# Kernel optimization log

Hardware: AMD Instinct MI355X
Metric: run time of the kernel (lower is better)

The kernel has to match this reference:

```python
import jax, jax.numpy as jnp
import numpy as np

# TT factorization of a 4096 -> 4096 linear layer
IN_SHAPE = (8, 8, 8, 8)    # input_tt_shape, prod = 4096
OUT_SHAPE = (8, 8, 8, 8)   # output_tt_shape, prod = 4096
RANKS = (1, 16, 16, 16, 1) # tt_ranks, len = n_dim + 1
N_DIM = len(IN_SHAPE)
BATCH = 2048
OUT_SIZE = int(np.prod(OUT_SHAPE))
IN_SIZE = int(np.prod(IN_SHAPE))


def setup_inputs() -> dict:
    key = jax.random.key(0)
    ks = jax.random.split(key, N_DIM + 1)
    x = jax.random.normal(ks[0], (BATCH, IN_SIZE), dtype=jnp.float32)
    inp = {"x": x}
    for i in range(N_DIM):
        rows = RANKS[i] * OUT_SHAPE[i]
        cols = IN_SHAPE[i] * RANKS[i + 1]
        # xavier_uniform scale, matching torch init statistics
        limit = float(np.sqrt(6.0 / (rows + cols)))
        inp[f"core{i}"] = jax.random.uniform(
            ks[i + 1], (rows, cols), minval=-limit, maxval=limit, dtype=jnp.float32
        )
    inp["bias"] = jnp.zeros((OUT_SIZE,), dtype=jnp.float32)
    return inp


def reference(x, core0, core1, core2, core3, bias):
    cores = [core0, core1, core2, core3]
    res = x  # [B, prod(IN_SHAPE)]
    # Sequential TT-core contraction, last mode first (faithful to torch loop)
    for k in range(N_DIM - 1, -1, -1):
        res = res.reshape(-1, IN_SHAPE[k])                     # [.., n_k]
        res = res.T                                            # [n_k, ..]
        res = res.reshape(RANKS[k + 1] * IN_SHAPE[k], -1)      # [r_{k+1}*n_k, ..]
        res = cores[k] @ res                                   # [r_k*m_k, ..]
    res = res.reshape(OUT_SIZE, -1).T                          # [B, prod(OUT_SHAPE)]
    return res + bias
```

## Files before the change

### kernel.cpp

```cpp
#include <hip/hip_runtime.h>
#include <hip/hip_bf16.h>
#include <stdint.h>


typedef __bf16 bf16_t;
typedef __bf16 bf16x8 __attribute__((ext_vector_type(8)));
typedef __bf16 bf16x4 __attribute__((ext_vector_type(4)));
typedef float floatx4 __attribute__((ext_vector_type(4)));

#define BATCH_N 2048
#define KD 4096
#define ND 4096

__device__ static inline void load_lds16(const void* g, void* l) {
    __builtin_amdgcn_global_load_lds(
        (const __attribute__((address_space(1))) void*)g,
        (__attribute__((address_space(3))) void*)l, 16, 0, 0);
}

__global__ __launch_bounds__(256) void prep0(const float* __restrict__ x,
                                             const float* __restrict__ c0,
                                             const float* __restrict__ c1,
                                             const float* __restrict__ c2,
                                             const float* __restrict__ c3,
                                             bf16_t* __restrict__ xb,
                                             float* __restrict__ Pg,
                                             float* __restrict__ Tg) {
    const int t = threadIdx.x;
    const int b = blockIdx.x;

    if (b < 4096) {
        int g = b * 256 + t;
        const float4* xv = (const float4*)x;
        float4 a = xv[g * 2];
        float4 c = xv[g * 2 + 1];
        bf16x8 o;
        o[0] = (bf16_t)a.x; o[1] = (bf16_t)a.y; o[2] = (bf16_t)a.z; o[3] = (bf16_t)a.w;
        o[4] = (bf16_t)c.x; o[5] = (bf16_t)c.y; o[6] = (bf16_t)c.z; o[7] = (bf16_t)c.w;
        ((bf16x8*)xb)[g] = o;
        return;
    }

    __shared__ float s0[128];
    __shared__ float s1[2048];

    if (b < 4160) {
        const int n01 = b - 4096, n0 = n01 >> 3, n1 = n01 & 7;
        if (t < 128) s0[t] = c0[(t >> 4) * 128 + n0 * 16 + (t & 15)];
        for (int i = t; i < 2048; i += 256) {
            int r1 = i >> 7, m1 = (i >> 4) & 7, r2 = i & 15;
            s1[i] = c1[(r1 * 8 + m1) * 128 + n1 * 16 + r2];
        }
        __syncthreads();
#pragma unroll
        for (int j = 0; j < 4; ++j) {
            int o = j * 256 + t, m01 = o >> 4, r2 = o & 15;
            int m0 = m01 >> 3, m1 = m01 & 7;
            float s = 0.f;
#pragma unroll
            for (int r1 = 0; r1 < 16; ++r1)
                s += s0[m0 * 16 + r1] * s1[r1 * 128 + m1 * 16 + r2];
            Pg[n01 * 1024 + o] = s;
        }
        return;
    }

    {
        const int m23 = b - 4160, m2 = m23 >> 3, m3 = m23 & 7;
        if (t < 128) s0[t] = c3[((t >> 3) * 8 + m3) * 8 + (t & 7)];
        for (int i = t; i < 2048; i += 256) {
            int r2 = i >> 7, n2 = (i >> 4) & 7, r3 = i & 15;
            s1[i] = c2[(r2 * 8 + m2) * 128 + n2 * 16 + r3];
        }
        __syncthreads();
#pragma unroll
        for (int j = 0; j < 4; ++j) {
            int o = j * 256 + t, n23 = o >> 4, r2 = o & 15;
            int n2 = n23 >> 3, n3 = n23 & 7;
            float s = 0.f;
#pragma unroll
            for (int r3 = 0; r3 < 16; ++r3)
                s += s1[r2 * 128 + n2 * 16 + r3] * s0[r3 * 8 + n3];
            Tg[m23 * 1024 + o] = s;
        }
    }
}

__global__ __launch_bounds__(256) void build_w(const float* __restrict__ Pg,
                                               const float* __restrict__ Tg,
                                               bf16_t* __restrict__ W) {
    const int t = threadIdx.x;
    const int b = blockIdx.x;
    const int n01 = b & 63, q = b >> 6;
    const int cg = t & 15;
    const int mr = t >> 4;
    const float* Pb = Pg + n01 * 1024 + q * 256;

#pragma unroll 1
    for (int ms = 0; ms < 4; ++ms) {
        const int m23 = ms * 16 + mr;
        float Tr[4][16];
#pragma unroll
        for (int jj = 0; jj < 4; ++jj) {
            const float4* tp = (const float4*)(Tg + (m23 * 64 + cg * 4 + jj) * 16);
#pragma unroll
            for (int w = 0; w < 4; ++w) {
                float4 v = tp[w];
                Tr[jj][w * 4 + 0] = v.x;
                Tr[jj][w * 4 + 1] = v.y;
                Tr[jj][w * 4 + 2] = v.z;
                Tr[jj][w * 4 + 3] = v.w;
            }
        }
#pragma unroll 4
        for (int ml = 0; ml < 16; ++ml) {
            float a0 = 0.f, a1 = 0.f, a2 = 0.f, a3 = 0.f;
#pragma unroll
            for (int r2 = 0; r2 < 16; ++r2) {
                float p = Pb[ml * 16 + r2];
                a0 += p * Tr[0][r2];
                a1 += p * Tr[1][r2];
                a2 += p * Tr[2][r2];
                a3 += p * Tr[3][r2];
            }
            bf16x4 o;
            o[0] = (bf16_t)a0; o[1] = (bf16_t)a1; o[2] = (bf16_t)a2; o[3] = (bf16_t)a3;
            *(bf16x4*)(W + (size_t)((q * 16 + ml) * 64 + m23) * 4096 + n01 * 64 + cg * 4) = o;
        }
    }
}

__global__ __launch_bounds__(256, 2) void gemm_bt(const bf16_t* __restrict__ A,
                                                  const bf16_t* __restrict__ B,
                                                  const float* __restrict__ bias,
                                                  float* __restrict__ C) {
    __shared__ bf16_t As[128 * 64];
    __shared__ bf16_t Bs[128 * 64];
    const int t = threadIdx.x;
    const int bid = blockIdx.x;
    const int xcd = bid & 7, g8 = bid >> 3;
    const int bm = xcd * 2 + (g8 & 1);
    const int bn = g8 >> 1;
    const int lane = t & 63, wave = t >> 6;
    const int wm = wave >> 1, wn = wave & 1;

    const int srow = lane >> 3;
    const int lc = (lane & 7) ^ srow;
    const bf16_t* Agp = A + (size_t)(bm * 128 + wave * 8 + srow) * KD + lc * 8;
    const bf16_t* Bgp = B + (size_t)(bn * 128 + wave * 8 + srow) * KD + lc * 8;
    bf16_t* AsW = As + wave * 512;
    bf16_t* BsW = Bs + wave * 512;

    floatx4 acc[4][4];
    floatx4 zero = {0.f, 0.f, 0.f, 0.f};
#pragma unroll
    for (int i = 0; i < 4; ++i)
#pragma unroll
        for (int j = 0; j < 4; ++j) acc[i][j] = zero;

    const int fr = lane & 15;
    const int fc = lane >> 4;

    for (int k0 = 0; k0 < KD; k0 += 64) {
        __syncthreads();
#pragma unroll
        for (int j = 0; j < 4; ++j) {
            load_lds16(Agp + (size_t)(j * 32) * KD + k0, AsW + j * 2048);
            load_lds16(Bgp + (size_t)(j * 32) * KD + k0, BsW + j * 2048);
        }
        __syncthreads();

#pragma unroll
        for (int kk = 0; kk < 2; ++kk) {
            const int pA = (fc + kk * 4) ^ (fr & 7);
            bf16x8 af[4], bf[4];
#pragma unroll
            for (int im = 0; im < 4; ++im)
                af[im] = *(const bf16x8*)(As + (wm * 64 + im * 16 + fr) * 64 + pA * 8);
#pragma unroll
            for (int in = 0; in < 4; ++in)
                bf[in] = *(const bf16x8*)(Bs + (wn * 64 + in * 16 + fr) * 64 + pA * 8);
#pragma unroll
            for (int im = 0; im < 4; ++im)
#pragma unroll
                for (int in = 0; in < 4; ++in)
                    acc[im][in] = __builtin_amdgcn_mfma_f32_16x16x32_bf16(
                        af[im], bf[in], acc[im][in], 0, 0, 0);
        }
    }

    const int rl = lane >> 4, cl = lane & 15;
    const size_t rbase = (size_t)bm * 128 + wm * 64;
    const int cbase = bn * 128 + wn * 64;
#pragma unroll
    for (int im = 0; im < 4; ++im) {
#pragma unroll
        for (int in = 0; in < 4; ++in) {
            int col = cbase + in * 16 + cl;
            float bv = bias[col];
#pragma unroll
            for (int r = 0; r < 4; ++r) {
                size_t row = rbase + im * 16 + rl * 4 + r;
                C[row * ND + col] = acc[im][in][r] + bv;
            }
        }
    }
}

extern "C" void kernel_launch(void* const* d_in, const int* in_sizes, int n_in,
                              void* d_out, int out_size, void* d_ws, size_t ws_size,
                              hipStream_t stream) {
    const float* x  = (const float*)d_in[0];
    const float* c0 = (const float*)d_in[1];
    const float* c1 = (const float*)d_in[2];
    const float* c2 = (const float*)d_in[3];
    const float* c3 = (const float*)d_in[4];
    const float* bias = (const float*)d_in[5];
    float* out = (float*)d_out;

    char* ws = (char*)d_ws;
    bf16_t* Xb = (bf16_t*)ws;
    bf16_t* W  = (bf16_t*)(ws + (16u << 20));

    float* Pg = (float*)d_out;
    float* Tg = Pg + 64 * 1024;

    prep0<<<4224, 256, 0, stream>>>(x, c0, c1, c2, c3, Xb, Pg, Tg);
    build_w<<<256, 256, 0, stream>>>(Pg, Tg, W);
    gemm_bt<<<512, 256, 0, stream>>>(Xb, W, bias, out);
}
```

Baseline: 177.5 us.

## Triple-buffer GEMM with 128x256 tiles, 8 waves and prefetch two stages ahead

Replaces the single-buffered 128x128 GEMM with a 512-thread, 128x256-tile kernel. It uses three LDS stages and issues the global-to-LDS loads two k-steps ahead, waiting with explicit vmcnt and a barrier so loads overlap the MFMA work. MFMA sections are wrapped in s_setprio to favour compute. The larger tile raises operand reuse and halves the grid to 256 blocks. In exchange it uses 144 KB of LDS per block, which limits occupancy, and relies on hand-tuned waitcnt counts for correctness.

```diff
diff --git a/kernel.cpp b/kernel.cpp
--- a/kernel.cpp
+++ b/kernel.cpp
@@ -130,26 +130,24 @@
     }
 }
 
-__global__ __launch_bounds__(256, 2) void gemm_bt(const bf16_t* __restrict__ A,
-                                                  const bf16_t* __restrict__ B,
-                                                  const float* __restrict__ bias,
-                                                  float* __restrict__ C) {
-    __shared__ bf16_t As[128 * 64];
-    __shared__ bf16_t Bs[128 * 64];
+__global__ __launch_bounds__(512, 2) void gemm_bt2(const bf16_t* __restrict__ A,
+                                                   const bf16_t* __restrict__ B,
+                                                   const float* __restrict__ bias,
+                                                   float* __restrict__ C) {
+    __shared__ bf16_t smem[3][24576];
     const int t = threadIdx.x;
     const int bid = blockIdx.x;
-    const int xcd = bid & 7, g8 = bid >> 3;
-    const int bm = xcd * 2 + (g8 & 1);
-    const int bn = g8 >> 1;
+    const int xcd = bid & 7, idx = bid >> 3;
+    const int bm = xcd * 2 + (idx & 1);
+    const int bn = idx >> 1;
     const int lane = t & 63, wave = t >> 6;
-    const int wm = wave >> 1, wn = wave & 1;
-
-    const int srow = lane >> 3;
-    const int lc = (lane & 7) ^ srow;
-    const bf16_t* Agp = A + (size_t)(bm * 128 + wave * 8 + srow) * KD + lc * 8;
-    const bf16_t* Bgp = B + (size_t)(bn * 128 + wave * 8 + srow) * KD + lc * 8;
-    bf16_t* AsW = As + wave * 512;
-    bf16_t* BsW = Bs + wave * 512;
+    const int wm = wave >> 2, wn = wave & 3;
+
+    const int srow = t >> 3;
+    const int lc = (t & 7) ^ (srow & 7);
+    const bf16_t* Ag = A + (size_t)(bm * 128 + srow) * KD + lc * 8;
+    const bf16_t* Bg = B + (size_t)(bn * 256 + srow) * KD + lc * 8;
+    const int woff = wave * 512;
 
     floatx4 acc[4][4];
     floatx4 zero = {0.f, 0.f, 0.f, 0.f};
@@ -161,37 +159,67 @@
     const int fr = lane & 15;
     const int fc = lane >> 4;
 
-    for (int k0 = 0; k0 < KD; k0 += 64) {
-        __syncthreads();
-#pragma unroll
-        for (int j = 0; j < 4; ++j) {
-            load_lds16(Agp + (size_t)(j * 32) * KD + k0, AsW + j * 2048);
-            load_lds16(Bgp + (size_t)(j * 32) * KD + k0, BsW + j * 2048);
-        }
-        __syncthreads();
-
+#pragma unroll
+    for (int kt = 0; kt < 2; ++kt) {
+        bf16_t* bb = &smem[kt][0];
+        const size_t ko = (size_t)kt * 64;
+#pragma unroll
+        for (int c = 0; c < 2; ++c)
+            load_lds16(Ag + (size_t)c * 64 * KD + ko, bb + c * 4096 + woff);
+#pragma unroll
+        for (int c = 0; c < 4; ++c)
+            load_lds16(Bg + (size_t)c * 64 * KD + ko, bb + 8192 + c * 4096 + woff);
+    }
+    asm volatile("s_waitcnt vmcnt(6)\n\ts_barrier" ::: "memory");
+
+    int cur = 0;
+#pragma unroll 1
+    for (int kt = 0; kt < 64; ++kt) {
+        if (kt < 62) {
+            int nb = cur + 2; if (nb >= 3) nb -= 3;
+            bf16_t* bb = &smem[nb][0];
+            const size_t ko = (size_t)(kt + 2) * 64;
+#pragma unroll
+            for (int c = 0; c < 2; ++c)
+                load_lds16(Ag + (size_t)c * 64 * KD + ko, bb + c * 4096 + woff);
+#pragma unroll
+            for (int c = 0; c < 4; ++c)
+                load_lds16(Bg + (size_t)c * 64 * KD + ko, bb + 8192 + c * 4096 + woff);
+        }
+
+        const bf16_t* Ab = &smem[cur][0];
+        const bf16_t* Bb = &smem[cur][8192];
 #pragma unroll
         for (int kk = 0; kk < 2; ++kk) {
             const int pA = (fc + kk * 4) ^ (fr & 7);
             bf16x8 af[4], bf[4];
 #pragma unroll
             for (int im = 0; im < 4; ++im)
-                af[im] = *(const bf16x8*)(As + (wm * 64 + im * 16 + fr) * 64 + pA * 8);
+                af[im] = *(const bf16x8*)(Ab + (wm * 64 + im * 16 + fr) * 64 + pA * 8);
 #pragma unroll
             for (int in = 0; in < 4; ++in)
-                bf[in] = *(const bf16x8*)(Bs + (wn * 64 + in * 16 + fr) * 64 + pA * 8);
+                bf[in] = *(const bf16x8*)(Bb + (wn * 64 + in * 16 + fr) * 64 + pA * 8);
+            __builtin_amdgcn_s_setprio(1);
 #pragma unroll
             for (int im = 0; im < 4; ++im)
 #pragma unroll
                 for (int in = 0; in < 4; ++in)
                     acc[im][in] = __builtin_amdgcn_mfma_f32_16x16x32_bf16(
                         af[im], bf[in], acc[im][in], 0, 0, 0);
-        }
+            __builtin_amdgcn_s_setprio(0);
+        }
+
+        if (kt < 62) {
+            asm volatile("s_waitcnt vmcnt(6) lgkmcnt(0)\n\ts_barrier" ::: "memory");
+        } else if (kt == 62) {
+            asm volatile("s_waitcnt vmcnt(0) lgkmcnt(0)\n\ts_barrier" ::: "memory");
+        }
+        cur = (cur == 2) ? 0 : cur + 1;
     }
 
     const int rl = lane >> 4, cl = lane & 15;
     const size_t rbase = (size_t)bm * 128 + wm * 64;
-    const int cbase = bn * 128 + wn * 64;
+    const int cbase = bn * 256 + wn * 64;
 #pragma unroll
     for (int im = 0; im < 4; ++im) {
 #pragma unroll
@@ -227,5 +255,5 @@
 
     prep0<<<4224, 256, 0, stream>>>(x, c0, c1, c2, c3, Xb, Pg, Tg);
     build_w<<<256, 256, 0, stream>>>(Pg, Tg, W);
-    gemm_bt<<<512, 256, 0, stream>>>(Xb, W, bias, out);
-}
+    gemm_bt2<<<256, 512, 0, stream>>>(Xb, W, bias, out);
+}
```

Result: faster. 171.4 us (-3.4%).
